# Kernel tuning notes

Hardware: AMD Instinct MI355X
Metric: run time of the kernel (lower is better)

Reference implementation:

```python
import jax, jax.numpy as jnp
import numpy as np

E, H, M = 1024, 16, 256
B, S = 2, 2048
D = E // H
SCALE = D ** -0.5


def setup_inputs() -> dict:
    key = jax.random.key(0)
    ks = jax.random.split(key, 10)
    p = 0.02
    return {
        "x": jax.random.normal(ks[0], (B, S, E), jnp.float32),
        "Wq": jax.random.normal(ks[1], (E, E), jnp.float32) * p,
        "bq": jax.random.normal(ks[2], (E,), jnp.float32) * p,
        "Wk": jax.random.normal(ks[3], (E, E), jnp.float32) * p,
        "bk": jax.random.normal(ks[4], (E,), jnp.float32) * p,
        "Wv": jax.random.normal(ks[5], (E, E), jnp.float32) * p,
        "bv": jax.random.normal(ks[6], (E,), jnp.float32) * p,
        "Wo": jax.random.normal(ks[7], (E, E), jnp.float32) * p,
        "bo": jax.random.normal(ks[8], (E,), jnp.float32) * p,
        "memory_state": jax.random.normal(ks[9], (M, E), jnp.float32) * p,
    }


def reference(x, Wq, bq, Wk, bk, Wv, bv, Wo, bo, memory_state):
    b, s, e = x.shape
    # QKV projections (torch Linear: y = x W^T + b), split heads -> [b,h,s,d]
    q = (x @ Wq.T + bq).reshape(b, s, H, D).transpose(0, 2, 1, 3)
    k = (x @ Wk.T + bk).reshape(b, s, H, D).transpose(0, 2, 1, 3)
    v = (x @ Wv.T + bv).reshape(b, s, H, D).transpose(0, 2, 1, 3)
    # full self-attention (eval mode: dropout is identity)
    attn = jax.nn.softmax(jnp.einsum("bhqd,bhkd->bhqk", q, k) * SCALE, axis=-1)
    attn_out = jnp.einsum("bhqk,bhkd->bhqd", attn, v)
    attn_out = attn_out.transpose(0, 2, 1, 3).reshape(b, s, e)
    # memory-read cross-attention on raw x against compressed memory [M,E]
    mem_w = jax.nn.softmax(jnp.einsum("bse,me->bsm", x, memory_state) * SCALE, axis=-1)
    mem_out = jnp.einsum("bsm,me->bse", mem_w, memory_state)
    out = attn_out + 0.5 * mem_out
    return out @ Wo.T + bo
```

## Files before the change

kernel.cpp:

```cpp
#include <hip/hip_runtime.h>
#include <cstdint>
#include <cstddef>


typedef __bf16 bf16;
typedef bf16  bf16x8 __attribute__((ext_vector_type(8)));
typedef bf16  bf16x4 __attribute__((ext_vector_type(4)));
typedef float f32x4  __attribute__((ext_vector_type(4)));
typedef float f32x16 __attribute__((ext_vector_type(16)));
typedef int   i32x4  __attribute__((ext_vector_type(4)));
typedef int   i32x2  __attribute__((ext_vector_type(2)));

#define B_DIM 2
#define S_DIM 2048
#define E_DIM 1024
#define H_DIM 16
#define D_DIM 64
#define M_DIM 256
#define NROW  (B_DIM * S_DIM)
#define C1 0.18033688011112042f

#define MFMA32(a, b, c) __builtin_amdgcn_mfma_f32_32x32x16_bf16((a), (b), (c), 0, 0, 0)

__device__ __forceinline__ f32x16 zero16()
{
    f32x16 z;
#pragma unroll
    for (int i = 0; i < 16; ++i) z[i] = 0.f;
    return z;
}

__device__ __forceinline__ void async_cp16(const bf16* g, bf16* l)
{
    __builtin_amdgcn_global_load_lds(
        (const __attribute__((address_space(1))) void*)g,
        (__attribute__((address_space(3))) void*)l, 16, 0, 0);
}

__global__ void __launch_bounds__(256)
conv_all(const float* __restrict__ x,  const float* __restrict__ Wq,
         const float* __restrict__ Wk, const float* __restrict__ Wv,
         const float* __restrict__ Wo, const float* __restrict__ mem,
         bf16* __restrict__ xb,  bf16* __restrict__ Wqb,
         bf16* __restrict__ Wkb, bf16* __restrict__ Wvb,
         bf16* __restrict__ Wob, bf16* __restrict__ memb,
         bf16* __restrict__ memt)
{
    for (int t = blockIdx.x * 256 + threadIdx.x; t < 1081344; t += 2048 * 256) {
        const float* src; bf16* dst; int off; bool is_mem = false;
        if      (t <  524288) { src = x;   dst = xb;   off = t; }
        else if (t <  655360) { src = Wq;  dst = Wqb;  off = t - 524288; }
        else if (t <  786432) { src = Wk;  dst = Wkb;  off = t - 655360; }
        else if (t <  917504) { src = Wv;  dst = Wvb;  off = t - 786432; }
        else if (t < 1048576) { src = Wo;  dst = Wob;  off = t - 917504; }
        else                  { src = mem; dst = memb; off = t - 1048576; is_mem = true; }
        const float4* p = (const float4*)src + (size_t)off * 2;
        float4 a = p[0], b = p[1];
        bf16x8 o;
        o[0] = (bf16)a.x; o[1] = (bf16)a.y; o[2] = (bf16)a.z; o[3] = (bf16)a.w;
        o[4] = (bf16)b.x; o[5] = (bf16)b.y; o[6] = (bf16)b.z; o[7] = (bf16)b.w;
        *(bf16x8*)(dst + (size_t)off * 8) = o;
        if (is_mem) {
            int r = off >> 7, c0 = (off & 127) * 8;
            float h[8] = {a.x, a.y, a.z, a.w, b.x, b.y, b.z, b.w};
#pragma unroll
            for (int j = 0; j < 8; ++j)
                memt[(size_t)(c0 + j) * M_DIM + r] = (bf16)(0.5f * h[j]);
        }
    }
}

struct GemmAcc { f32x4 a[4][4]; };

__device__ __forceinline__ void
gemm_core(const bf16* __restrict__ A, const bf16* __restrict__ Bm,
          int K, int m0, int n0, bf16* As, bf16* Bs, GemmAcc& R)
{
    const int tid  = threadIdx.x;
    const int lane = tid & 63;
    const int wave = tid >> 6;
    const int quad = lane >> 4;
    const int l16  = lane & 15;
    const int wm   = (wave >> 1) * 64;
    const int wn   = (wave & 1) * 64;

#pragma unroll
    for (int i = 0; i < 4; ++i)
#pragma unroll
        for (int j = 0; j < 4; ++j)
            R.a[i][j] = f32x4{0.f, 0.f, 0.f, 0.f};

    int s_c0  = wave * 128 + lane;
    int s_r0  = s_c0 >> 2;
    int s_k0  = (s_c0 & 3) ^ ((s_r0 >> 1) & 3);
    int s_c1  = s_c0 + 64;
    int s_r1  = s_c1 >> 2;
    int s_k1  = (s_c1 & 3) ^ ((s_r1 >> 1) & 3);
    const bf16* gA0 = A  + (size_t)(m0 + s_r0) * K + s_k0 * 8;
    const bf16* gA1 = A  + (size_t)(m0 + s_r1) * K + s_k1 * 8;
    const bf16* gB0 = Bm + (size_t)(n0 + s_r0) * K + s_k0 * 8;
    const bf16* gB1 = Bm + (size_t)(n0 + s_r1) * K + s_k1 * 8;

#define STAGE(buf, k0)                                                     \
    do {                                                                   \
        async_cp16(gA0 + (k0), &As[(buf) * 4096 + wave * 1024]);           \
        async_cp16(gA1 + (k0), &As[(buf) * 4096 + wave * 1024 + 512]);     \
        async_cp16(gB0 + (k0), &Bs[(buf) * 4096 + wave * 1024]);           \
        async_cp16(gB1 + (k0), &Bs[(buf) * 4096 + wave * 1024 + 512]);     \
    } while (0)

    STAGE(0, 0);
    int buf = 0;
    for (int k0 = 0; k0 < K; k0 += 32) {
        __syncthreads();
        if (k0 + 32 < K) STAGE(buf ^ 1, k0 + 32);

        const bf16* Ab = As + buf * 4096;
        const bf16* Bb = Bs + buf * 4096;
        bf16x8 af[4], bfr[4];
#pragma unroll
        for (int mi = 0; mi < 4; ++mi) {
            int m    = wm + mi * 16 + l16;
            int slot = quad ^ ((m >> 1) & 3);
            af[mi]   = *(const bf16x8*)(&Ab[(m * 4 + slot) * 8]);
        }
#pragma unroll
        for (int ni = 0; ni < 4; ++ni) {
            int n    = wn + ni * 16 + l16;
            int slot = quad ^ ((n >> 1) & 3);
            bfr[ni]  = *(const bf16x8*)(&Bb[(n * 4 + slot) * 8]);
        }
#pragma unroll
        for (int mi = 0; mi < 4; ++mi)
#pragma unroll
            for (int ni = 0; ni < 4; ++ni)
                R.a[mi][ni] = __builtin_amdgcn_mfma_f32_16x16x32_bf16(
                    af[mi], bfr[ni], R.a[mi][ni], 0, 0, 0);
        buf ^= 1;
    }
#undef STAGE
}

__global__ void __launch_bounds__(256, 3)
gemm_qkvl(const bf16* __restrict__ A,
          const bf16* __restrict__ Wq, const bf16* __restrict__ Wk,
          const bf16* __restrict__ Wv, const bf16* __restrict__ memb,
          const float* __restrict__ bq, const float* __restrict__ bk,
          const float* __restrict__ bv,
          bf16* __restrict__ q, bf16* __restrict__ k,
          bf16* __restrict__ vt, bf16* __restrict__ lg)
{
    __shared__ __align__(16) bf16 As[2 * 4096];
    __shared__ __align__(16) bf16 Bs[2 * 4096];
    const int lid  = blockIdx.x;
    const int xcd  = lid & 7;
    const int idx  = lid >> 3;
    const int mloc = idx / 26;
    const int nn   = idx - mloc * 26;
    const int m0   = (mloc * 8 + xcd) * 128;
    const int widx = (nn < 24) ? (nn >> 3) : 3;
    const int n0   = (nn < 24) ? (nn & 7) * 128 : (nn - 24) * 128;
    const bf16*  Bm = (widx == 0) ? Wq : (widx == 1) ? Wk :
                      (widx == 2) ? Wv : memb;
    GemmAcc R;
    gemm_core(A, Bm, E_DIM, m0, n0, As, Bs, R);

    const int lane = threadIdx.x & 63, wave = threadIdx.x >> 6;
    const int quad = lane >> 4, l16 = lane & 15;
    const int wm = (wave >> 1) * 64, wn = (wave & 1) * 64;

    if (widx == 0 || widx == 1) {
        bf16* C = (widx == 0) ? q : k;
        const float* bi = (widx == 0) ? bq : bk;
        float scale = (widx == 0) ? C1 : 1.0f;
#pragma unroll
        for (int ni = 0; ni < 4; ++ni) {
            int col  = n0 + wn + ni * 16 + l16;
            float bb = bi[col];
#pragma unroll
            for (int mi = 0; mi < 4; ++mi)
#pragma unroll
                for (int r = 0; r < 4; ++r) {
                    int rowg = m0 + wm + mi * 16 + quad * 4 + r;
                    C[(size_t)rowg * E_DIM + col] =
                        (bf16)((R.a[mi][ni][r] + bb) * scale);
                }
        }
    } else if (widx == 2) {
#pragma unroll
        for (int ni = 0; ni < 4; ++ni) {
            int col = n0 + wn + ni * 16 + l16;
            float bb = bv[col];
#pragma unroll
            for (int mi = 0; mi < 4; ++mi) {
                int row0 = m0 + wm + mi * 16 + quad * 4;
                int bidx = row0 >> 11, s = row0 & 2047;
                bf16x4 pk;
#pragma unroll
                for (int r = 0; r < 4; ++r) pk[r] = (bf16)(R.a[mi][ni][r] + bb);
                *(bf16x4*)(&vt[((size_t)(bidx * H_DIM) * 64 + col) * S_DIM + s]) = pk;
            }
        }
    } else {
#pragma unroll
        for (int ni = 0; ni < 4; ++ni) {
            int col = n0 + wn + ni * 16 + l16;
#pragma unroll
            for (int mi = 0; mi < 4; ++mi)
#pragma unroll
                for (int r = 0; r < 4; ++r) {
                    int rowg = m0 + wm + mi * 16 + quad * 4 + r;
                    lg[(size_t)rowg * M_DIM + col] = (bf16)R.a[mi][ni][r];
                }
        }
    }
}

__global__ void __launch_bounds__(256, 2)
gemm_out64(const bf16* __restrict__ A, const bf16* __restrict__ Bm,
           const float* __restrict__ bias, float* __restrict__ C)
{
    __shared__ __align__(16) bf16 As[2 * 2048];
    __shared__ __align__(16) bf16 Bs[2 * 4096];
    const int tid  = threadIdx.x;
    const int lane = tid & 63;
    const int wave = tid >> 6;
    const int quad = lane >> 4;
    const int l16  = lane & 15;
    const int wm   = (wave >> 1) * 32;
    const int wn   = (wave & 1) * 64;
    const int lid  = blockIdx.x;
    const int xcd  = lid & 7;
    const int idx  = lid >> 3;
    const int mloc = idx >> 3;
    const int nn   = idx & 7;
    const int m0   = (mloc * 8 + xcd) * 64;
    const int n0   = nn * 128;
    const int K    = E_DIM;

    f32x4 acc[2][4];
#pragma unroll
    for (int i = 0; i < 2; ++i)
#pragma unroll
        for (int j = 0; j < 4; ++j) acc[i][j] = f32x4{0.f, 0.f, 0.f, 0.f};

    int a_s  = wave * 64 + lane;
    int a_r  = a_s >> 2;
    int a_k  = (a_s & 3) ^ ((a_r >> 1) & 3);
    int b_s0 = wave * 128 + lane;
    int b_r0 = b_s0 >> 2;
    int b_k0 = (b_s0 & 3) ^ ((b_r0 >> 1) & 3);
    int b_s1 = b_s0 + 64;
    int b_r1 = b_s1 >> 2;
    int b_k1 = (b_s1 & 3) ^ ((b_r1 >> 1) & 3);
    const bf16* gA  = A  + (size_t)(m0 + a_r) * K + a_k * 8;
    const bf16* gB0 = Bm + (size_t)(n0 + b_r0) * K + b_k0 * 8;
    const bf16* gB1 = Bm + (size_t)(n0 + b_r1) * K + b_k1 * 8;

#define STAGE64(buf, k0)                                                   \
    do {                                                                   \
        async_cp16(gA  + (k0), &As[(buf) * 2048 + wave * 512]);            \
        async_cp16(gB0 + (k0), &Bs[(buf) * 4096 + wave * 1024]);           \
        async_cp16(gB1 + (k0), &Bs[(buf) * 4096 + wave * 1024 + 512]);     \
    } while (0)

    STAGE64(0, 0);
    int buf = 0;
    for (int k0 = 0; k0 < K; k0 += 32) {
        __syncthreads();
        if (k0 + 32 < K) STAGE64(buf ^ 1, k0 + 32);
        const bf16* Ab = As + buf * 2048;
        const bf16* Bb = Bs + buf * 4096;
        bf16x8 af[2], bfr[4];
#pragma unroll
        for (int mi = 0; mi < 2; ++mi) {
            int m    = wm + mi * 16 + l16;
            int slot = quad ^ ((m >> 1) & 3);
            af[mi]   = *(const bf16x8*)(&Ab[(m * 4 + slot) * 8]);
        }
#pragma unroll
        for (int ni = 0; ni < 4; ++ni) {
            int n    = wn + ni * 16 + l16;
            int slot = quad ^ ((n >> 1) & 3);
            bfr[ni]  = *(const bf16x8*)(&Bb[(n * 4 + slot) * 8]);
        }
#pragma unroll
        for (int mi = 0; mi < 2; ++mi)
#pragma unroll
            for (int ni = 0; ni < 4; ++ni)
                acc[mi][ni] = __builtin_amdgcn_mfma_f32_16x16x32_bf16(
                    af[mi], bfr[ni], acc[mi][ni], 0, 0, 0);
        buf ^= 1;
    }
#undef STAGE64

#pragma unroll
    for (int ni = 0; ni < 4; ++ni) {
        int col  = n0 + wn + ni * 16 + l16;
        float bb = bias[col];
#pragma unroll
        for (int mi = 0; mi < 2; ++mi)
#pragma unroll
            for (int r = 0; r < 4; ++r) {
                int rowg = m0 + wm + mi * 16 + quad * 4 + r;
                C[(size_t)rowg * E_DIM + col] = acc[mi][ni][r] + bb;
            }
    }
}

__global__ void __launch_bounds__(256, 2)
flash_attn(const bf16* __restrict__ q, const bf16* __restrict__ k,
           const bf16* __restrict__ vt, const bf16* __restrict__ lg,
           const bf16* __restrict__ memt, bf16* __restrict__ outc)
{
    __shared__ __align__(16) bf16 Ks[2 * 4096];
    __shared__ __align__(16) bf16 Vs[2 * 4096];
    const int tid  = threadIdx.x;
    const int lane = tid & 63;
    const int wave = tid >> 6;
    const int hi   = lane >> 5;
    const int l32  = lane & 31;
    const int lid = blockIdx.x;
    const int xcd = lid & 7;
    const int kk  = lid >> 3;
    const int qt  = kk & 15;
    const int p   = ((kk >> 4) << 3) | xcd;
    const int b   = p >> 4;
    const int h   = p & 15;
    const int q0  = qt * 128 + wave * 32;

    const bf16* qb = q  + (size_t)(b * S_DIM + q0) * E_DIM + h * D_DIM;
    const bf16* kb = k  + (size_t)(b * S_DIM) * E_DIM + h * D_DIM;
    const bf16* vb = vt + (size_t)(b * H_DIM + h) * D_DIM * S_DIM;

    const int s_s0 = wave * 128 + lane;
    const int s_r0 = s_s0 >> 3;
    const int s_g0 = (s_s0 & 7) ^ (s_r0 & 7);
    const int s_s1 = s_s0 + 64;
    const int s_r1 = s_s1 >> 3;
    const int s_g1 = (s_s1 & 7) ^ (s_r1 & 7);
    const bf16* gK0 = kb + (size_t)s_r0 * E_DIM + s_g0 * 8;
    const bf16* gK1 = kb + (size_t)s_r1 * E_DIM + s_g1 * 8;
    const bf16* gV0 = vb + (size_t)s_r0 * S_DIM + s_g0 * 8;
    const bf16* gV1 = vb + (size_t)s_r1 * S_DIM + s_g1 * 8;

    const int kd0 = wave * 1024 + lane * 8;
    const int v00 = s_r0 * 64 + (((s_g0 & ~1)    ) ^ (s_r0 & 7)) * 8 + (s_g0 & 1) * 4;
    const int v01 = s_r0 * 64 + (((s_g0 & ~1) | 1) ^ (s_r0 & 7)) * 8 + (s_g0 & 1) * 4;
    const int v10 = s_r1 * 64 + (((s_g1 & ~1)    ) ^ (s_r1 & 7)) * 8 + (s_g1 & 1) * 4;
    const int v11 = s_r1 * 64 + (((s_g1 & ~1) | 1) ^ (s_r1 & 7)) * 8 + (s_g1 & 1) * 4;

    bf16x8 qfr[4];
#pragma unroll
    for (int c = 0; c < 4; ++c)
        qfr[c] = *(const bf16x8*)(qb + (size_t)l32 * E_DIM + c * 16 + hi * 8);

    bf16x8 vones;
#pragma unroll
    for (int j = 0; j < 8; ++j) vones[j] = (bf16)1.0f;

    f32x16 o_acc0 = zero16(), o_acc1 = zero16(), osum = zero16();

    {
        i32x4 rK0 = *(const i32x4*)(gK0);
        i32x4 rK1 = *(const i32x4*)(gK1);
        i32x4 rV0 = *(const i32x4*)(gV0);
        i32x4 rV1 = *(const i32x4*)(gV1);
        *(i32x4*)(&Ks[kd0])       = rK0;
        *(i32x4*)(&Ks[kd0 + 512]) = rK1;
        *(i32x2*)(&Vs[v00]) = i32x2{rV0[0], rV0[1]};
        *(i32x2*)(&Vs[v01]) = i32x2{rV0[2], rV0[3]};
        *(i32x2*)(&Vs[v10]) = i32x2{rV1[0], rV1[1]};
        *(i32x2*)(&Vs[v11]) = i32x2{rV1[2], rV1[3]};
    }
    __syncthreads();

    int buf = 0;
    for (int kt = 0; kt < S_DIM; kt += 64) {
        const bool pre = (kt + 64 < S_DIM);
        i32x4 nK0, nK1, nV0, nV1;
        if (pre) {
            const size_t ko = (size_t)(kt + 64) * E_DIM;
            nK0 = *(const i32x4*)(gK0 + ko);
            nK1 = *(const i32x4*)(gK1 + ko);
            nV0 = *(const i32x4*)(gV0 + (kt + 64));
            nV1 = *(const i32x4*)(gV1 + (kt + 64));
        }
        const bf16* Kb = Ks + buf * 4096;
        const bf16* Vb = Vs + buf * 4096;

        f32x16 sc0 = zero16(), sc1 = zero16();
        __builtin_amdgcn_s_setprio(1);
#pragma unroll
        for (int c = 0; c < 4; ++c) {
            const int cc  = c * 2 + hi;
            const int swz = (cc ^ (l32 & 7)) * 8;
            bf16x8 kf0 = *(const bf16x8*)(&Kb[l32 * 64 + swz]);
            bf16x8 kf1 = *(const bf16x8*)(&Kb[(32 + l32) * 64 + swz]);
            sc0 = MFMA32(kf0, qfr[c], sc0);
            sc1 = MFMA32(kf1, qfr[c], sc1);
        }
        __builtin_amdgcn_s_setprio(0);

        bf16x8 ap[4];
#pragma unroll
        for (int kc = 0; kc < 4; ++kc) {
            const f32x16 sct = (kc < 2) ? sc0 : sc1;
            const int base = (kc & 1) * 8;
#pragma unroll
            for (int j = 0; j < 8; ++j)
                ap[kc][j] = (bf16)exp2f(sct[base + j]);
        }

        __builtin_amdgcn_s_setprio(1);
#pragma unroll
        for (int kc = 0; kc < 4; ++kc) {
            const int swz = ((kc * 2 + hi) ^ (l32 & 7)) * 8;
            bf16x8 vf0 = *(const bf16x8*)(&Vb[l32 * 64 + swz]);
            bf16x8 vf1 = *(const bf16x8*)(&Vb[(32 + l32) * 64 + swz]);
            o_acc0 = MFMA32(ap[kc], vf0, o_acc0);
            o_acc1 = MFMA32(ap[kc], vf1, o_acc1);
            osum   = MFMA32(ap[kc], vones, osum);
        }
        __builtin_amdgcn_s_setprio(0);

        if (pre) {
            const int bo = (buf ^ 1) * 4096;
            *(i32x4*)(&Ks[bo + kd0])       = nK0;
            *(i32x4*)(&Ks[bo + kd0 + 512]) = nK1;
            *(i32x2*)(&Vs[bo + v00]) = i32x2{nV0[0], nV0[1]};
            *(i32x2*)(&Vs[bo + v01]) = i32x2{nV0[2], nV0[3]};
            *(i32x2*)(&Vs[bo + v10]) = i32x2{nV1[0], nV1[1]};
            *(i32x2*)(&Vs[bo + v11]) = i32x2{nV1[2], nV1[3]};
        }
        __syncthreads();
        buf ^= 1;
    }

    float linv[16];
#pragma unroll
    for (int r = 0; r < 16; ++r) linv[r] = 1.f / osum[r];

    const bf16* Pr = lg   + (size_t)(b * S_DIM + q0) * M_DIM;
    const bf16* Mt = memt + (size_t)(h * D_DIM) * M_DIM;
    f32x16 macc0 = zero16(), macc1 = zero16(), msum = zero16();
#pragma unroll
    for (int mc = 0; mc < 16; ++mc) {
        bf16x8 raw = *(const bf16x8*)(Pr + (size_t)l32 * M_DIM + mc * 16 + hi * 8);
        bf16x8 epv;
#pragma unroll
        for (int j = 0; j < 8; ++j) epv[j] = (bf16)exp2f(C1 * (float)raw[j]);
        bf16x8 bm0 = *(const bf16x8*)(Mt + (size_t)l32 * M_DIM        + mc * 16 + hi * 8);
        bf16x8 bm1 = *(const bf16x8*)(Mt + (size_t)(32 + l32) * M_DIM + mc * 16 + hi * 8);
        macc0 = MFMA32(epv, bm0, macc0);
        macc1 = MFMA32(epv, bm1, macc1);
        msum  = MFMA32(epv, vones, msum);
    }

    bf16* ob = outc + (size_t)(b * S_DIM + q0) * E_DIM + h * D_DIM;
#pragma unroll
    for (int r = 0; r < 16; ++r) {
        const int qrow = (r & 3) + 8 * (r >> 2) + 4 * hi;
        const float mi = 1.f / msum[r];
        ob[(size_t)qrow * E_DIM + l32]      = (bf16)(o_acc0[r] * linv[r] + macc0[r] * mi);
        ob[(size_t)qrow * E_DIM + 32 + l32] = (bf16)(o_acc1[r] * linv[r] + macc1[r] * mi);
    }
}

extern "C" void kernel_launch(void* const* d_in, const int* in_sizes, int n_in,
                              void* d_out, int out_size, void* d_ws, size_t ws_size,
                              hipStream_t stream)
{
    (void)in_sizes; (void)n_in; (void)out_size; (void)ws_size;
    const float* x   = (const float*)d_in[0];
    const float* Wq  = (const float*)d_in[1];
    const float* bq  = (const float*)d_in[2];
    const float* Wk  = (const float*)d_in[3];
    const float* bk  = (const float*)d_in[4];
    const float* Wv  = (const float*)d_in[5];
    const float* bv  = (const float*)d_in[6];
    const float* Wo  = (const float*)d_in[7];
    const float* bo  = (const float*)d_in[8];
    const float* mem = (const float*)d_in[9];
    float* out = (float*)d_out;

    bf16* w = (bf16*)d_ws;
    const size_t NE = (size_t)NROW * E_DIM;
    const size_t EE = (size_t)E_DIM * E_DIM;
    bf16* xb      = w;
    bf16* q_ws    = w + NE;
    bf16* k_ws    = w + 2 * NE;
    bf16* Wqb     = w + 3 * NE;
    bf16* Wkb     = Wqb + EE;
    bf16* Wvb     = Wkb + EE;
    bf16* Wob     = Wvb + EE;
    bf16* memb    = Wob + EE;
    bf16* lg_ws   = memb + (size_t)M_DIM * E_DIM;
    bf16* memt_ws = lg_ws + (size_t)NROW * M_DIM;
    bf16* vt_ws = (bf16*)d_out;

    dim3 blk(256);

    conv_all<<<dim3(2048), blk, 0, stream>>>(
        x, Wq, Wk, Wv, Wo, mem, xb, Wqb, Wkb, Wvb, Wob, memb, memt_ws);

    gemm_qkvl<<<dim3(832), blk, 0, stream>>>(
        xb, Wqb, Wkb, Wvb, memb, bq, bk, bv, q_ws, k_ws, vt_ws, lg_ws);

    flash_attn<<<dim3(512), blk, 0, stream>>>(
        q_ws, k_ws, vt_ws, lg_ws, memt_ws, q_ws);

    gemm_out64<<<dim3(512), blk, 0, stream>>>(
        q_ws, Wob, bo, out);
}
```

Baseline: 214.5 us.

## Split flash attention over two KV halves with a separate combine kernel

Replaces the single flash-attention kernel with a split-KV version: 1024 blocks each process half of the key/value sequence and write unnormalized fp32 partial outputs and row sums to workspace, then a combine kernel sums the halves, normalizes, and adds the memory-read attention. This doubles the grid so more of the GPU's compute units are busy during attention. In exchange it adds an extra launch and fp32 partial-result traffic through global memory. It falls back to the old kernel if the workspace is too small.

```diff
diff --git a/kernel.cpp b/kernel.cpp
--- a/kernel.cpp
+++ b/kernel.cpp
@@ -19,6 +19,7 @@
 #define M_DIM 256
 #define NROW  (B_DIM * S_DIM)
 #define C1 0.18033688011112042f
+#define PLANES 131072
 
 #define MFMA32(a, b, c) __builtin_amdgcn_mfma_f32_32x32x16_bf16((a), (b), (c), 0, 0, 0)
 
@@ -467,11 +468,225 @@
     }
 }
 
+__global__ void __launch_bounds__(256, 4)
+flash_partial(const bf16* __restrict__ q, const bf16* __restrict__ k,
+              const bf16* __restrict__ vt,
+              float* __restrict__ po, float* __restrict__ ps)
+{
+    __shared__ __align__(16) bf16 Ks[2 * 4096];
+    __shared__ __align__(16) bf16 Vs[2 * 4096];
+    const int tid  = threadIdx.x;
+    const int lane = tid & 63;
+    const int wave = tid >> 6;
+    const int hi   = lane >> 5;
+    const int l32  = lane & 31;
+    const int lid = blockIdx.x;
+    const int xcd = lid & 7;
+    const int kk  = lid >> 3;
+    const int qt  = kk & 15;
+    const int ks  = (kk >> 4) & 1;
+    const int p   = ((kk >> 5) << 3) | xcd;
+    const int b   = p >> 4;
+    const int h   = p & 15;
+    const int q0  = qt * 128 + wave * 32;
+    const int pq  = p * 16 + qt;
+    const int kv0 = ks * 1024;
+
+    const bf16* qb = q  + (size_t)(b * S_DIM + q0) * E_DIM + h * D_DIM;
+    const bf16* kb = k  + (size_t)(b * S_DIM) * E_DIM + h * D_DIM;
+    const bf16* vb = vt + (size_t)(b * H_DIM + h) * D_DIM * S_DIM;
+
+    const int s_s0 = wave * 128 + lane;
+    const int s_r0 = s_s0 >> 3;
+    const int s_g0 = (s_s0 & 7) ^ (s_r0 & 7);
+    const int s_s1 = s_s0 + 64;
+    const int s_r1 = s_s1 >> 3;
+    const int s_g1 = (s_s1 & 7) ^ (s_r1 & 7);
+    const bf16* gK0 = kb + (size_t)(kv0 + s_r0) * E_DIM + s_g0 * 8;
+    const bf16* gK1 = kb + (size_t)(kv0 + s_r1) * E_DIM + s_g1 * 8;
+    const bf16* gV0 = vb + (size_t)s_r0 * S_DIM + kv0 + s_g0 * 8;
+    const bf16* gV1 = vb + (size_t)s_r1 * S_DIM + kv0 + s_g1 * 8;
+
+    const int kd0 = wave * 1024 + lane * 8;
+    const int v00 = s_r0 * 64 + (((s_g0 & ~1)    ) ^ (s_r0 & 7)) * 8 + (s_g0 & 1) * 4;
+    const int v01 = s_r0 * 64 + (((s_g0 & ~1) | 1) ^ (s_r0 & 7)) * 8 + (s_g0 & 1) * 4;
+    const int v10 = s_r1 * 64 + (((s_g1 & ~1)    ) ^ (s_r1 & 7)) * 8 + (s_g1 & 1) * 4;
+    const int v11 = s_r1 * 64 + (((s_g1 & ~1) | 1) ^ (s_r1 & 7)) * 8 + (s_g1 & 1) * 4;
+
+    bf16x8 qfr[4];
+#pragma unroll
+    for (int c = 0; c < 4; ++c)
+        qfr[c] = *(const bf16x8*)(qb + (size_t)l32 * E_DIM + c * 16 + hi * 8);
+
+    bf16x8 vones;
+#pragma unroll
+    for (int j = 0; j < 8; ++j) vones[j] = (bf16)1.0f;
+
+    f32x16 o_acc0 = zero16(), o_acc1 = zero16(), osum = zero16();
+
+    {
+        i32x4 rK0 = *(const i32x4*)(gK0);
+        i32x4 rK1 = *(const i32x4*)(gK1);
+        i32x4 rV0 = *(const i32x4*)(gV0);
+        i32x4 rV1 = *(const i32x4*)(gV1);
+        *(i32x4*)(&Ks[kd0])       = rK0;
+        *(i32x4*)(&Ks[kd0 + 512]) = rK1;
+        *(i32x2*)(&Vs[v00]) = i32x2{rV0[0], rV0[1]};
+        *(i32x2*)(&Vs[v01]) = i32x2{rV0[2], rV0[3]};
+        *(i32x2*)(&Vs[v10]) = i32x2{rV1[0], rV1[1]};
+        *(i32x2*)(&Vs[v11]) = i32x2{rV1[2], rV1[3]};
+    }
+    __syncthreads();
+
+    int buf = 0;
+    for (int kt = 0; kt < 1024; kt += 64) {
+        const bool pre = (kt + 64 < 1024);
+        i32x4 nK0, nK1, nV0, nV1;
+        if (pre) {
+            const size_t ko = (size_t)(kt + 64) * E_DIM;
+            nK0 = *(const i32x4*)(gK0 + ko);
+            nK1 = *(const i32x4*)(gK1 + ko);
+            nV0 = *(const i32x4*)(gV0 + (kt + 64));
+            nV1 = *(const i32x4*)(gV1 + (kt + 64));
+        }
+        const bf16* Kb = Ks + buf * 4096;
+        const bf16* Vb = Vs + buf * 4096;
+
+        f32x16 sc0 = zero16(), sc1 = zero16();
+        __builtin_amdgcn_s_setprio(1);
+#pragma unroll
+        for (int c = 0; c < 4; ++c) {
+            const int cc  = c * 2 + hi;
+            const int swz = (cc ^ (l32 & 7)) * 8;
+            bf16x8 kf0 = *(const bf16x8*)(&Kb[l32 * 64 + swz]);
+            bf16x8 kf1 = *(const bf16x8*)(&Kb[(32 + l32) * 64 + swz]);
+            sc0 = MFMA32(kf0, qfr[c], sc0);
+            sc1 = MFMA32(kf1, qfr[c], sc1);
+        }
+        __builtin_amdgcn_s_setprio(0);
+
+        bf16x8 ap[4];
+#pragma unroll
+        for (int kc = 0; kc < 4; ++kc) {
+            const f32x16 sct = (kc < 2) ? sc0 : sc1;
+            const int base = (kc & 1) * 8;
+#pragma unroll
+            for (int j = 0; j < 8; ++j)
+                ap[kc][j] = (bf16)exp2f(sct[base + j]);
+        }
+
+        __builtin_amdgcn_s_setprio(1);
+#pragma unroll
+        for (int kc = 0; kc < 4; ++kc) {
+            const int swz = ((kc * 2 + hi) ^ (l32 & 7)) * 8;
+            bf16x8 vf0 = *(const bf16x8*)(&Vb[l32 * 64 + swz]);
+            bf16x8 vf1 = *(const bf16x8*)(&Vb[(32 + l32) * 64 + swz]);
+            o_acc0 = MFMA32(ap[kc], vf0, o_acc0);
+            o_acc1 = MFMA32(ap[kc], vf1, o_acc1);
+            osum   = MFMA32(ap[kc], vones, osum);
+        }
+        __builtin_amdgcn_s_setprio(0);
+
+        if (pre) {
+            const int bo = (buf ^ 1) * 4096;
+            *(i32x4*)(&Ks[bo + kd0])       = nK0;
+            *(i32x4*)(&Ks[bo + kd0 + 512]) = nK1;
+            *(i32x2*)(&Vs[bo + v00]) = i32x2{nV0[0], nV0[1]};
+            *(i32x2*)(&Vs[bo + v01]) = i32x2{nV0[2], nV0[3]};
+            *(i32x2*)(&Vs[bo + v10]) = i32x2{nV1[0], nV1[1]};
+            *(i32x2*)(&Vs[bo + v11]) = i32x2{nV1[2], nV1[3]};
+        }
+        __syncthreads();
+        buf ^= 1;
+    }
+
+    const size_t ll = ((size_t)pq * 4 + wave) * 64 + lane;
+#pragma unroll
+    for (int r = 0; r < 16; ++r)
+        po[(size_t)(r * 2 + ks) * PLANES + ll] = o_acc0[r];
+#pragma unroll
+    for (int r = 0; r < 16; ++r)
+        po[(size_t)((16 + r) * 2 + ks) * PLANES + ll] = o_acc1[r];
+    if (l32 == 0) {
+        const size_t sb = ((((size_t)pq * 4 + wave) * 2 + hi) * 16) * 2 + ks;
+#pragma unroll
+        for (int r = 0; r < 16; ++r) ps[sb + (size_t)r * 2] = osum[r];
+    }
+}
+
+__global__ void __launch_bounds__(256, 2)
+flash_combine(const float* __restrict__ po, const float* __restrict__ ps,
+              const bf16* __restrict__ lg, const bf16* __restrict__ memt,
+              bf16* __restrict__ outc)
+{
+    const int tid  = threadIdx.x;
+    const int lane = tid & 63;
+    const int wave = tid >> 6;
+    const int hi   = lane >> 5;
+    const int l32  = lane & 31;
+    const int pq   = blockIdx.x;
+    const int p    = pq >> 4;
+    const int qt   = pq & 15;
+    const int b    = p >> 4;
+    const int h    = p & 15;
+    const int q0   = qt * 128 + wave * 32;
+
+    const size_t ll = ((size_t)pq * 4 + wave) * 64 + lane;
+    f32x16 o0, o1, osum;
+#pragma unroll
+    for (int r = 0; r < 16; ++r)
+        o0[r] = po[(size_t)(r * 2) * PLANES + ll]
+              + po[(size_t)(r * 2 + 1) * PLANES + ll];
+#pragma unroll
+    for (int r = 0; r < 16; ++r)
+        o1[r] = po[(size_t)((16 + r) * 2) * PLANES + ll]
+              + po[(size_t)((16 + r) * 2 + 1) * PLANES + ll];
+    {
+        const size_t sb = ((((size_t)pq * 4 + wave) * 2 + hi) * 16) * 2;
+#pragma unroll
+        for (int r = 0; r < 16; ++r)
+            osum[r] = ps[sb + (size_t)r * 2] + ps[sb + (size_t)r * 2 + 1];
+    }
+
+    float linv[16];
+#pragma unroll
+    for (int r = 0; r < 16; ++r) linv[r] = 1.f / osum[r];
+
+    bf16x8 vones;
+#pragma unroll
+    for (int j = 0; j < 8; ++j) vones[j] = (bf16)1.0f;
+
+    const bf16* Pr = lg   + (size_t)(b * S_DIM + q0) * M_DIM;
+    const bf16* Mt = memt + (size_t)(h * D_DIM) * M_DIM;
+    f32x16 macc0 = zero16(), macc1 = zero16(), msum = zero16();
+#pragma unroll
+    for (int mc = 0; mc < 16; ++mc) {
+        bf16x8 raw = *(const bf16x8*)(Pr + (size_t)l32 * M_DIM + mc * 16 + hi * 8);
+        bf16x8 epv;
+#pragma unroll
+        for (int j = 0; j < 8; ++j) epv[j] = (bf16)exp2f(C1 * (float)raw[j]);
+        bf16x8 bm0 = *(const bf16x8*)(Mt + (size_t)l32 * M_DIM        + mc * 16 + hi * 8);
+        bf16x8 bm1 = *(const bf16x8*)(Mt + (size_t)(32 + l32) * M_DIM + mc * 16 + hi * 8);
+        macc0 = MFMA32(epv, bm0, macc0);
+        macc1 = MFMA32(epv, bm1, macc1);
+        msum  = MFMA32(epv, vones, msum);
+    }
+
+    bf16* ob = outc + (size_t)(b * S_DIM + q0) * E_DIM + h * D_DIM;
+#pragma unroll
+    for (int r = 0; r < 16; ++r) {
+        const int qrow = (r & 3) + 8 * (r >> 2) + 4 * hi;
+        const float mi = 1.f / msum[r];
+        ob[(size_t)qrow * E_DIM + l32]      = (bf16)(o0[r] * linv[r] + macc0[r] * mi);
+        ob[(size_t)qrow * E_DIM + 32 + l32] = (bf16)(o1[r] * linv[r] + macc1[r] * mi);
+    }
+}
+
 extern "C" void kernel_launch(void* const* d_in, const int* in_sizes, int n_in,
                               void* d_out, int out_size, void* d_ws, size_t ws_size,
                               hipStream_t stream)
 {
-    (void)in_sizes; (void)n_in; (void)out_size; (void)ws_size;
+    (void)in_sizes; (void)n_in; (void)out_size;
     const float* x   = (const float*)d_in[0];
     const float* Wq  = (const float*)d_in[1];
     const float* bq  = (const float*)d_in[2];
@@ -497,7 +712,14 @@
     bf16* memb    = Wob + EE;
     bf16* lg_ws   = memb + (size_t)M_DIM * E_DIM;
     bf16* memt_ws = lg_ws + (size_t)NROW * M_DIM;
+    bf16* ws_end  = memt_ws + (size_t)E_DIM * M_DIM;
     bf16* vt_ws = (bf16*)d_out;
+
+    float* po = (float*)ws_end;
+    float* ps = po + (size_t)64 * PLANES;
+    size_t needed = (size_t)((char*)(ps + (size_t)512 * 4 * 2 * 16 * 2)
+                             - (char*)d_ws);
+    const bool split = (ws_size >= needed);
 
     dim3 blk(256);
 
@@ -507,8 +729,15 @@
     gemm_qkvl<<<dim3(832), blk, 0, stream>>>(
         xb, Wqb, Wkb, Wvb, memb, bq, bk, bv, q_ws, k_ws, vt_ws, lg_ws);
 
-    flash_attn<<<dim3(512), blk, 0, stream>>>(
-        q_ws, k_ws, vt_ws, lg_ws, memt_ws, q_ws);
+    if (split) {
+        flash_partial<<<dim3(1024), blk, 0, stream>>>(
+            q_ws, k_ws, vt_ws, po, ps);
+        flash_combine<<<dim3(512), blk, 0, stream>>>(
+            po, ps, lg_ws, memt_ws, q_ws);
+    } else {
+        flash_attn<<<dim3(512), blk, 0, stream>>>(
+            q_ws, k_ws, vt_ws, lg_ws, memt_ws, q_ws);
+    }
 
     gemm_out64<<<dim3(512), blk, 0, stream>>>(
         q_ws, Wob, bo, out);
```

New measurement: 255.1 us. 1.19x slower.
